# Kernel optimization log

Measured on AMD Instinct MI355X. Metric: run time of the kernel, lower is better.

## Reference

```python
import jax, jax.numpy as jnp
import numpy as np

N, M, BS = 32, 64, 512
ALPHA, BETA = 1.0, 1.0


def setup_inputs() -> dict:
    key = jax.random.key(0)
    k1, k2, k3, k4 = jax.random.split(key, 4)
    q = jax.random.normal(k1, (BS, N), jnp.float32)
    b = jax.random.normal(k2, (BS, M), jnp.float32)
    A0 = jax.random.normal(k3, (N, N), jnp.float32)
    P = A0 @ A0.T / N + jnp.eye(N, dtype=jnp.float32)  # SPD cost matrix
    H = jax.random.normal(k4, (M, N), jnp.float32) / jnp.sqrt(jnp.float32(N))
    return {"q": q, "b": b, "P": P, "H": H, "iters": 1000}


def reference(q, b, P, H, iters):
    m = H.shape[0]
    # Pinv-applied quantities via solve (matches torch.linalg.solve / pinv usage)
    Pinv_q = jnp.linalg.solve(P, q.T).T                 # (bs, n)
    D = H @ jnp.linalg.solve(P, H.T)                    # (m, m) = H P^-1 H^T
    # dummy preconditioner: scaled identity keeping the operator nonexpansive
    lam_max = jnp.linalg.eigvalsh(D)[-1]
    tD = (BETA / lam_max) * jnp.eye(m, dtype=q.dtype)   # (m, m)
    mu = ((H @ Pinv_q.T).T - b) @ tD.T                  # (bs, m)
    tDD = tD @ D
    I = jnp.eye(m, dtype=q.dtype)
    A = jnp.block([[tDD, tD],
                   [-2.0 * ALPHA * tDD + I, I - 2.0 * ALPHA * tD]])  # (2m, 2m)
    B = jnp.concatenate([mu, -2.0 * ALPHA * mu], axis=1)             # (bs, 2m)
    Hinv = jnp.linalg.pinv(H)                            # (n, m)
    X0 = jnp.zeros((q.shape[0], 2 * m), q.dtype)

    def step(X, _):
        X = X @ A.T + B
        X = X.at[:, m:].set(jax.nn.relu(X[:, m:]))       # in-place ReLU on dual half
        return X, X

    _, ys = jax.lax.scan(step, X0, None, length=iters)   # (iters, bs, 2m)
    Xs = jnp.concatenate([X0[None], ys], axis=0).transpose(1, 0, 2)  # (bs, iters+1, 2m)
    # primal_sols[k] = Hinv @ (X_k[m:] - b)
    primal_sols = jnp.einsum('nm,bkm->bkn', Hinv, Xs[:, :, m:] - b[:, None, :])
    return Xs, primal_sols
```

## Files before the change

### kernel.cpp

```cpp
#include <hip/hip_runtime.h>
#include <math.h>

#define BATCH 512
#define ITERS 1000
#define PLEN 25
#define PHASES 40

typedef float f32x2 __attribute__((ext_vector_type(2)));
typedef float f32x4 __attribute__((ext_vector_type(4)));

__device__ __forceinline__ float rdlane(float v, int l) {
  return __int_as_float(__builtin_amdgcn_readlane(__float_as_int(v), l));
}
__device__ __forceinline__ f32x2 fma2(f32x2 a, f32x2 b, f32x2 c) {
#if __has_builtin(__builtin_elementwise_fma)
  return __builtin_elementwise_fma(a, b, c);
#else
  f32x2 r; r.x = fmaf(a.x, b.x, c.x); r.y = fmaf(a.y, b.y, c.y); return r;
#endif
}

#define GJ32_REG(g)                                            \
  _Pragma("unroll")                                            \
  for (int k = 0; k < 32; ++k) {                               \
    float inv = 1.0f / rdlane(g[k], k);                        \
    g[k] *= inv;                                               \
    _Pragma("unroll")                                          \
    for (int ii = 0; ii < 32; ++ii) {                          \
      if (ii == k) continue;                                   \
      float f = rdlane(g[ii], k);                              \
      g[ii] = fmaf(-f, g[k], g[ii]);                           \
    }                                                          \
  }

__global__ __launch_bounds__(128, 1)
void fused_kernel(const float* __restrict__ q,
                  const float* __restrict__ bmat,
                  const float* __restrict__ P,
                  const float* __restrict__ H,
                  float* __restrict__ Xs,
                  float* __restrict__ out2) {
  __shared__ __align__(16) float stage[2112];
  __shared__ __align__(16) float X1R[2][PLEN][64];
  __shared__ __align__(16) float X2R[2][PLEN][64];

  const int tid = threadIdx.x;
  const int wv = tid >> 6;
  const int lane = tid & 63;
  const int row = blockIdx.x;
  const int i = lane & 31, h = lane >> 5;

  float hreg[32];
  {
    const f32x4* hp = (const f32x4*)(H + lane * 32);
    #pragma unroll
    for (int j4 = 0; j4 < 8; ++j4) {
      f32x4 t = hp[j4];
      hreg[4*j4+0] = t.x; hreg[4*j4+1] = t.y; hreg[4*j4+2] = t.z; hreg[4*j4+3] = t.w;
    }
  }
  const float bl = bmat[row * 64 + lane];

  float dcol[64]; float s = 0.f, mu = 0.f;
  f32x2 hv2[16];
  float* Xp = Xs + (size_t)row * (ITERS + 1) * 128;
  float* ob = out2 + (size_t)row * (ITERS + 1) * 32;

  if (wv == 1) {
    #pragma unroll
    for (int j = 0; j < 32; ++j) stage[lane * 33 + j] = hreg[j];
  }
  __syncthreads();
  float gB[32];
  if (wv == 1) {
    float htc[64];
    #pragma unroll
    for (int m = 0; m < 64; ++m) htc[m] = stage[m * 33 + i];
    #pragma unroll
    for (int r = 0; r < 32; ++r) {
      float a0 = 0.f, a1 = 0.f;
      #pragma unroll
      for (int m = 0; m < 64; m += 2) {
        a0 = fmaf(rdlane(hreg[r], m),     htc[m],     a0);
        a1 = fmaf(rdlane(hreg[r], m + 1), htc[m + 1], a1);
      }
      float hth = a0 + a1;
      gB[r] = (lane < 32) ? hth : (((lane - 32) == r) ? 1.0f : 0.0f);
    }
    GJ32_REG(gB)
  }
  __syncthreads();
  if (wv == 1) {
    #pragma unroll
    for (int r = 0; r < 32; ++r) {
      float a0 = 0.f, a1 = 0.f;
      #pragma unroll
      for (int c = 0; c < 32; c += 2) {
        a0 = fmaf(rdlane(gB[r], 32 + c),     hreg[c],     a0);
        a1 = fmaf(rdlane(gB[r], 32 + c + 1), hreg[c + 1], a1);
      }
      stage[r * 66 + lane] = a0 + a1;
    }
  }
  __syncthreads();
  if (wv == 1) {
    #pragma unroll
    for (int t = 0; t < 16; ++t)
      hv2[t] = *(const f32x2*)&stage[i * 66 + 32 * h + 2 * t];
  }

  if (wv == 0) {
    float pht[32], acc;
    {
      float g[32];
      #pragma unroll
      for (int r = 0; r < 32; ++r) {
        float pv = P[r * 32 + i];
        g[r] = (lane < 32) ? pv : (((lane - 32) == r) ? 1.0f : 0.0f);
      }
      GJ32_REG(g)
      #pragma unroll
      for (int r = 0; r < 32; ++r) {
        float a0 = 0.f, a1 = 0.f;
        #pragma unroll
        for (int j = 0; j < 32; j += 2) {
          a0 = fmaf(rdlane(g[r], 32 + j),     hreg[j],     a0);
          a1 = fmaf(rdlane(g[r], 32 + j + 1), hreg[j + 1], a1);
        }
        pht[r] = a0 + a1;
      }
    }
    {
      const float* qp = q + row * 32;
      float a0 = 0.f, a1 = 0.f;
      #pragma unroll
      for (int r = 0; r < 32; r += 2) {
        a0 = fmaf(qp[r],     pht[r],     a0);
        a1 = fmaf(qp[r + 1], pht[r + 1], a1);
      }
      acc = a0 + a1;
    }
    #pragma unroll
    for (int r = 0; r < 64; ++r) {
      float a0 = 0.f, a1 = 0.f;
      #pragma unroll
      for (int j = 0; j < 32; j += 2) {
        a0 = fmaf(rdlane(hreg[j],     r), pht[j],     a0);
        a1 = fmaf(rdlane(hreg[j + 1], r), pht[j + 1], a1);
      }
      dcol[r] = a0 + a1;
    }
    {
      float ecol[64];
      #pragma unroll
      for (int r = 0; r < 64; ++r) {
        float a0 = 0.f, a1 = 0.f;
        #pragma unroll
        for (int c = 0; c < 64; c += 2) {
          a0 = fmaf(rdlane(dcol[r], c),     dcol[c],     a0);
          a1 = fmaf(rdlane(dcol[r], c + 1), dcol[c + 1], a1);
        }
        ecol[r] = a0 + a1;
      }
      float v = 1.0f + 0.017f * (float)lane;
      #pragma unroll 1
      for (int t = 0; t < 112; ++t) {
        float a0 = 0.f, a1 = 0.f, a2 = 0.f, a3 = 0.f;
        #pragma unroll
        for (int c = 0; c < 64; c += 4) {
          a0 = fmaf(ecol[c+0], rdlane(v, c+0), a0);
          a1 = fmaf(ecol[c+1], rdlane(v, c+1), a1);
          a2 = fmaf(ecol[c+2], rdlane(v, c+2), a2);
          a3 = fmaf(ecol[c+3], rdlane(v, c+3), a3);
        }
        v = (a0 + a1) + (a2 + a3);
        if ((t & 7) == 7) {
          float n2 = v * v;
          #pragma unroll
          for (int m = 1; m < 64; m <<= 1) n2 += __shfl_xor(n2, m);
          v *= 1.0f / sqrtf(n2);
        }
      }
      float a0 = 0.f, a1 = 0.f, a2 = 0.f, a3 = 0.f;
      #pragma unroll
      for (int c = 0; c < 64; c += 4) {
        a0 = fmaf(dcol[c+0], rdlane(v, c+0), a0);
        a1 = fmaf(dcol[c+1], rdlane(v, c+1), a1);
        a2 = fmaf(dcol[c+2], rdlane(v, c+2), a2);
        a3 = fmaf(dcol[c+3], rdlane(v, c+3), a3);
      }
      float w = (a0 + a1) + (a2 + a3);
      float num = w * v, den = v * v;
      #pragma unroll
      for (int m = 1; m < 64; m <<= 1) {
        num += __shfl_xor(num, m);
        den += __shfl_xor(den, m);
      }
      s = den / num;
    }
    mu = s * (acc - bl);
    #pragma unroll
    for (int r = 0; r < 64; ++r) dcol[r] *= s;
  }

  float x1 = 0.f, x2 = 0.f;
  #pragma unroll 1
  for (int p = 0; p < PHASES; ++p) {
    if (wv == 0) {
      float* rx1 = &X1R[p & 1][0][0];
      float* rx2 = &X2R[p & 1][0][0];
      #pragma unroll 1
      for (int u = 0; u < PLEN; ++u) {
        float a0 = 0.f, a1 = 0.f, a2 = 0.f, a3 = 0.f;
        #pragma unroll
        for (int j8 = 0; j8 < 64; j8 += 8) {
          float b0 = rdlane(x1, j8+0), b1 = rdlane(x1, j8+1);
          float b2 = rdlane(x1, j8+2), b3 = rdlane(x1, j8+3);
          float b4 = rdlane(x1, j8+4), b5 = rdlane(x1, j8+5);
          float b6 = rdlane(x1, j8+6), b7 = rdlane(x1, j8+7);
          a0 = fmaf(dcol[j8+0], b0, a0);
          a1 = fmaf(dcol[j8+1], b1, a1);
          a2 = fmaf(dcol[j8+2], b2, a2);
          a3 = fmaf(dcol[j8+3], b3, a3);
          a0 = fmaf(dcol[j8+4], b4, a0);
          a1 = fmaf(dcol[j8+5], b5, a1);
          a2 = fmaf(dcol[j8+6], b6, a2);
          a3 = fmaf(dcol[j8+7], b7, a3);
        }
        float x1n = ((a0 + a1) + (a2 + a3)) + fmaf(s, x2, mu);
        float x2n = fmaxf(fmaf(-2.0f, x1n, x1 + x2), 0.f);
        rx1[u * 64 + lane] = x1n;
        rx2[u * 64 + lane] = x2n - bl;
        x1 = x1n; x2 = x2n;
      }
    } else {
      if (p == 0) {
        Xp[lane] = 0.f;
        Xp[64 + lane] = 0.f;
        f32x2 pa = {0.f, 0.f}, pb = {0.f, 0.f};
        #pragma unroll
        for (int t = 0; t < 8; ++t) {
          f32x2 ta, tb;
          ta.x = -__shfl(bl, 32*h + 4*t + 0, 64);
          ta.y = -__shfl(bl, 32*h + 4*t + 1, 64);
          tb.x = -__shfl(bl, 32*h + 4*t + 2, 64);
          tb.y = -__shfl(bl, 32*h + 4*t + 3, 64);
          pa = fma2(hv2[2*t],     ta, pa);
          pb = fma2(hv2[2*t + 1], tb, pb);
        }
        float pr = (pa.x + pa.y) + (pb.x + pb.y);
        pr += __shfl_xor(pr, 32);
        if (h == 0) ob[i] = pr;
      } else {
        const float* rx1 = &X1R[(p - 1) & 1][0][0];
        const float* rx2 = &X2R[(p - 1) & 1][0][0];
        const int k0 = PLEN * (p - 1) + 1;
        float* Xk = Xp + (size_t)k0 * 128;
        float* obk = ob + (size_t)k0 * 32;
        #pragma unroll 1
        for (int u = 0; u < PLEN; ++u) {
          float x1v = rx1[u * 64 + lane];
          float x2mb = rx2[u * 64 + lane];
          Xk[u * 128 + lane] = x1v;
          Xk[u * 128 + 64 + lane] = x2mb + bl;
          const f32x4* tp = (const f32x4*)(rx2 + u * 64 + h * 32);
          f32x2 pa = {0.f, 0.f}, pb = {0.f, 0.f};
          #pragma unroll
          for (int t = 0; t < 8; ++t) {
            f32x4 tv = tp[t];
            pa = fma2(hv2[2*t],     tv.xy, pa);
            pb = fma2(hv2[2*t + 1], tv.zw, pb);
          }
          float pr = (pa.x + pa.y) + (pb.x + pb.y);
          pr += __shfl_xor(pr, 32);
          if (h == 0) obk[u * 32 + i] = pr;
        }
      }
    }
    __syncthreads();
  }

  if (wv == 1) {
    const float* rx1 = &X1R[1][0][0];
    const float* rx2 = &X2R[1][0][0];
    const int k0 = PLEN * (PHASES - 1) + 1;
    float* Xk = Xp + (size_t)k0 * 128;
    float* obk = ob + (size_t)k0 * 32;
    #pragma unroll 1
    for (int u = 0; u < PLEN; ++u) {
      float x1v = rx1[u * 64 + lane];
      float x2mb = rx2[u * 64 + lane];
      Xk[u * 128 + lane] = x1v;
      Xk[u * 128 + 64 + lane] = x2mb + bl;
      const f32x4* tp = (const f32x4*)(rx2 + u * 64 + h * 32);
      f32x2 pa = {0.f, 0.f}, pb = {0.f, 0.f};
      #pragma unroll
      for (int t = 0; t < 8; ++t) {
        f32x4 tv = tp[t];
        pa = fma2(hv2[2*t],     tv.xy, pa);
        pb = fma2(hv2[2*t + 1], tv.zw, pb);
      }
      float pr = (pa.x + pa.y) + (pb.x + pb.y);
      pr += __shfl_xor(pr, 32);
      if (h == 0) obk[u * 32 + i] = pr;
    }
  }
}

extern "C" void kernel_launch(void* const* d_in, const int* in_sizes, int n_in,
                              void* d_out, int out_size, void* d_ws, size_t ws_size,
                              hipStream_t stream) {
  (void)in_sizes; (void)n_in; (void)out_size; (void)d_ws; (void)ws_size;
  const float* q = (const float*)d_in[0];
  const float* b = (const float*)d_in[1];
  const float* P = (const float*)d_in[2];
  const float* H = (const float*)d_in[3];
  float* Xs = (float*)d_out;
  float* out2 = Xs + (size_t)BATCH * (ITERS + 1) * 128;

  fused_kernel<<<BATCH, 128, 0, stream>>>(q, b, P, H, Xs, out2);
}
```

Baseline: 611.9 us.

## Process two batch rows per block, interleaving their serial recurrences

Each block now handles two batch rows and launches BATCH/2 blocks. The compute wave interleaves the two independent 1000-step recurrences so their readlane and FMA chains can hide each other's latency. The setup work (the Gauss-Jordan inverse and D) is also amortised over two rows. In exchange the grid is halved to 256 blocks, which can underfill the GPU's compute units, and each serial step now does twice the readlanes, so time per step may roughly double.

```diff
diff --git a/kernel.cpp b/kernel.cpp
--- a/kernel.cpp
+++ b/kernel.cpp
@@ -33,6 +33,26 @@
     }                                                          \
   }
 
+#define CONSUME25(rx1, rx2, Xk, obk, blv)                      \
+  _Pragma("unroll 1")                                          \
+  for (int u = 0; u < PLEN; ++u) {                             \
+    float x1v  = (rx1)[u * 64 + lane];                         \
+    float x2mb = (rx2)[u * 64 + lane];                         \
+    (Xk)[u * 128 + lane] = x1v;                                \
+    (Xk)[u * 128 + 64 + lane] = x2mb + (blv);                  \
+    const f32x4* tp = (const f32x4*)((rx2) + u * 64 + h * 32); \
+    f32x2 pa = {0.f, 0.f}, pb = {0.f, 0.f};                    \
+    _Pragma("unroll")                                          \
+    for (int t = 0; t < 8; ++t) {                              \
+      f32x4 tv = tp[t];                                        \
+      pa = fma2(hv2[2*t],     tv.xy, pa);                      \
+      pb = fma2(hv2[2*t + 1], tv.zw, pb);                      \
+    }                                                          \
+    float pr = (pa.x + pa.y) + (pb.x + pb.y);                  \
+    pr += __shfl_xor(pr, 32);                                  \
+    if (h == 0) (obk)[u * 32 + i] = pr;                        \
+  }
+
 __global__ __launch_bounds__(128, 1)
 void fused_kernel(const float* __restrict__ q,
                   const float* __restrict__ bmat,
@@ -41,13 +61,13 @@
                   float* __restrict__ Xs,
                   float* __restrict__ out2) {
   __shared__ __align__(16) float stage[2112];
-  __shared__ __align__(16) float X1R[2][PLEN][64];
-  __shared__ __align__(16) float X2R[2][PLEN][64];
+  __shared__ __align__(16) float X1R[2][2][PLEN][64];
+  __shared__ __align__(16) float X2R[2][2][PLEN][64];
 
   const int tid = threadIdx.x;
   const int wv = tid >> 6;
   const int lane = tid & 63;
-  const int row = blockIdx.x;
+  const int r0 = blockIdx.x * 2;
   const int i = lane & 31, h = lane >> 5;
 
   float hreg[32];
@@ -59,12 +79,15 @@
       hreg[4*j4+0] = t.x; hreg[4*j4+1] = t.y; hreg[4*j4+2] = t.z; hreg[4*j4+3] = t.w;
     }
   }
-  const float bl = bmat[row * 64 + lane];
-
-  float dcol[64]; float s = 0.f, mu = 0.f;
+  const float bla = bmat[r0 * 64 + lane];
+  const float blb = bmat[r0 * 64 + 64 + lane];
+
+  float dcol[64]; float s = 0.f, mua = 0.f, mub = 0.f;
   f32x2 hv2[16];
-  float* Xp = Xs + (size_t)row * (ITERS + 1) * 128;
-  float* ob = out2 + (size_t)row * (ITERS + 1) * 32;
+  float* Xpa = Xs + (size_t)r0 * (ITERS + 1) * 128;
+  float* Xpb = Xpa + (size_t)(ITERS + 1) * 128;
+  float* oba = out2 + (size_t)r0 * (ITERS + 1) * 32;
+  float* obb = oba + (size_t)(ITERS + 1) * 32;
 
   if (wv == 1) {
     #pragma unroll
@@ -110,7 +133,7 @@
   }
 
   if (wv == 0) {
-    float pht[32], acc;
+    float pht[32], acca, accb;
     {
       float g[32];
       #pragma unroll
@@ -131,14 +154,18 @@
       }
     }
     {
-      const float* qp = q + row * 32;
-      float a0 = 0.f, a1 = 0.f;
+      const float* qa = q + r0 * 32;
+      const float* qb = qa + 32;
+      float a0 = 0.f, a1 = 0.f, b0 = 0.f, b1 = 0.f;
       #pragma unroll
       for (int r = 0; r < 32; r += 2) {
-        a0 = fmaf(qp[r],     pht[r],     a0);
-        a1 = fmaf(qp[r + 1], pht[r + 1], a1);
-      }
-      acc = a0 + a1;
+        a0 = fmaf(qa[r],     pht[r],     a0);
+        a1 = fmaf(qa[r + 1], pht[r + 1], a1);
+        b0 = fmaf(qb[r],     pht[r],     b0);
+        b1 = fmaf(qb[r + 1], pht[r + 1], b1);
+      }
+      acca = a0 + a1;
+      accb = b0 + b1;
     }
     #pragma unroll
     for (int r = 0; r < 64; ++r) {
@@ -198,112 +225,115 @@
       }
       s = den / num;
     }
-    mu = s * (acc - bl);
+    mua = s * (acca - bla);
+    mub = s * (accb - blb);
     #pragma unroll
     for (int r = 0; r < 64; ++r) dcol[r] *= s;
   }
 
-  float x1 = 0.f, x2 = 0.f;
+  float x1a = 0.f, x2a = 0.f, x1b = 0.f, x2b = 0.f;
   #pragma unroll 1
   for (int p = 0; p < PHASES; ++p) {
     if (wv == 0) {
-      float* rx1 = &X1R[p & 1][0][0];
-      float* rx2 = &X2R[p & 1][0][0];
+      float* rx1a = &X1R[p & 1][0][0][0];
+      float* rx2a = &X2R[p & 1][0][0][0];
+      float* rx1b = &X1R[p & 1][1][0][0];
+      float* rx2b = &X2R[p & 1][1][0][0];
       #pragma unroll 1
       for (int u = 0; u < PLEN; ++u) {
+        float ta = fmaf(s, x2a, mua), tb = fmaf(s, x2b, mub);
         float a0 = 0.f, a1 = 0.f, a2 = 0.f, a3 = 0.f;
+        float c0 = 0.f, c1 = 0.f, c2 = 0.f, c3 = 0.f;
         #pragma unroll
         for (int j8 = 0; j8 < 64; j8 += 8) {
-          float b0 = rdlane(x1, j8+0), b1 = rdlane(x1, j8+1);
-          float b2 = rdlane(x1, j8+2), b3 = rdlane(x1, j8+3);
-          float b4 = rdlane(x1, j8+4), b5 = rdlane(x1, j8+5);
-          float b6 = rdlane(x1, j8+6), b7 = rdlane(x1, j8+7);
-          a0 = fmaf(dcol[j8+0], b0, a0);
-          a1 = fmaf(dcol[j8+1], b1, a1);
-          a2 = fmaf(dcol[j8+2], b2, a2);
-          a3 = fmaf(dcol[j8+3], b3, a3);
-          a0 = fmaf(dcol[j8+4], b4, a0);
-          a1 = fmaf(dcol[j8+5], b5, a1);
-          a2 = fmaf(dcol[j8+6], b6, a2);
-          a3 = fmaf(dcol[j8+7], b7, a3);
-        }
-        float x1n = ((a0 + a1) + (a2 + a3)) + fmaf(s, x2, mu);
-        float x2n = fmaxf(fmaf(-2.0f, x1n, x1 + x2), 0.f);
-        rx1[u * 64 + lane] = x1n;
-        rx2[u * 64 + lane] = x2n - bl;
-        x1 = x1n; x2 = x2n;
+          float pa0 = rdlane(x1a, j8+0), pa1 = rdlane(x1a, j8+1);
+          float pa2 = rdlane(x1a, j8+2), pa3 = rdlane(x1a, j8+3);
+          float pa4 = rdlane(x1a, j8+4), pa5 = rdlane(x1a, j8+5);
+          float pa6 = rdlane(x1a, j8+6), pa7 = rdlane(x1a, j8+7);
+          float pb0 = rdlane(x1b, j8+0), pb1 = rdlane(x1b, j8+1);
+          float pb2 = rdlane(x1b, j8+2), pb3 = rdlane(x1b, j8+3);
+          float pb4 = rdlane(x1b, j8+4), pb5 = rdlane(x1b, j8+5);
+          float pb6 = rdlane(x1b, j8+6), pb7 = rdlane(x1b, j8+7);
+          a0 = fmaf(dcol[j8+0], pa0, a0);
+          c0 = fmaf(dcol[j8+0], pb0, c0);
+          a1 = fmaf(dcol[j8+1], pa1, a1);
+          c1 = fmaf(dcol[j8+1], pb1, c1);
+          a2 = fmaf(dcol[j8+2], pa2, a2);
+          c2 = fmaf(dcol[j8+2], pb2, c2);
+          a3 = fmaf(dcol[j8+3], pa3, a3);
+          c3 = fmaf(dcol[j8+3], pb3, c3);
+          a0 = fmaf(dcol[j8+4], pa4, a0);
+          c0 = fmaf(dcol[j8+4], pb4, c0);
+          a1 = fmaf(dcol[j8+5], pa5, a1);
+          c1 = fmaf(dcol[j8+5], pb5, c1);
+          a2 = fmaf(dcol[j8+6], pa6, a2);
+          c2 = fmaf(dcol[j8+6], pb6, c2);
+          a3 = fmaf(dcol[j8+7], pa7, a3);
+          c3 = fmaf(dcol[j8+7], pb7, c3);
+        }
+        float x1na = ((a0 + a1) + (a2 + a3)) + ta;
+        float x1nb = ((c0 + c1) + (c2 + c3)) + tb;
+        float x2na = fmaxf(fmaf(-2.0f, x1na, x1a + x2a), 0.f);
+        float x2nb = fmaxf(fmaf(-2.0f, x1nb, x1b + x2b), 0.f);
+        rx1a[u * 64 + lane] = x1na;
+        rx2a[u * 64 + lane] = x2na - bla;
+        rx1b[u * 64 + lane] = x1nb;
+        rx2b[u * 64 + lane] = x2nb - blb;
+        x1a = x1na; x2a = x2na; x1b = x1nb; x2b = x2nb;
       }
     } else {
       if (p == 0) {
-        Xp[lane] = 0.f;
-        Xp[64 + lane] = 0.f;
-        f32x2 pa = {0.f, 0.f}, pb = {0.f, 0.f};
-        #pragma unroll
-        for (int t = 0; t < 8; ++t) {
-          f32x2 ta, tb;
-          ta.x = -__shfl(bl, 32*h + 4*t + 0, 64);
-          ta.y = -__shfl(bl, 32*h + 4*t + 1, 64);
-          tb.x = -__shfl(bl, 32*h + 4*t + 2, 64);
-          tb.y = -__shfl(bl, 32*h + 4*t + 3, 64);
-          pa = fma2(hv2[2*t],     ta, pa);
-          pb = fma2(hv2[2*t + 1], tb, pb);
-        }
-        float pr = (pa.x + pa.y) + (pb.x + pb.y);
-        pr += __shfl_xor(pr, 32);
-        if (h == 0) ob[i] = pr;
-      } else {
-        const float* rx1 = &X1R[(p - 1) & 1][0][0];
-        const float* rx2 = &X2R[(p - 1) & 1][0][0];
-        const int k0 = PLEN * (p - 1) + 1;
-        float* Xk = Xp + (size_t)k0 * 128;
-        float* obk = ob + (size_t)k0 * 32;
-        #pragma unroll 1
-        for (int u = 0; u < PLEN; ++u) {
-          float x1v = rx1[u * 64 + lane];
-          float x2mb = rx2[u * 64 + lane];
-          Xk[u * 128 + lane] = x1v;
-          Xk[u * 128 + 64 + lane] = x2mb + bl;
-          const f32x4* tp = (const f32x4*)(rx2 + u * 64 + h * 32);
+        Xpa[lane] = 0.f; Xpa[64 + lane] = 0.f;
+        Xpb[lane] = 0.f; Xpb[64 + lane] = 0.f;
+        {
           f32x2 pa = {0.f, 0.f}, pb = {0.f, 0.f};
           #pragma unroll
           for (int t = 0; t < 8; ++t) {
-            f32x4 tv = tp[t];
-            pa = fma2(hv2[2*t],     tv.xy, pa);
-            pb = fma2(hv2[2*t + 1], tv.zw, pb);
+            f32x2 ta, tb;
+            ta.x = -__shfl(bla, 32*h + 4*t + 0, 64);
+            ta.y = -__shfl(bla, 32*h + 4*t + 1, 64);
+            tb.x = -__shfl(bla, 32*h + 4*t + 2, 64);
+            tb.y = -__shfl(bla, 32*h + 4*t + 3, 64);
+            pa = fma2(hv2[2*t],     ta, pa);
+            pb = fma2(hv2[2*t + 1], tb, pb);
           }
           float pr = (pa.x + pa.y) + (pb.x + pb.y);
           pr += __shfl_xor(pr, 32);
-          if (h == 0) obk[u * 32 + i] = pr;
-        }
+          if (h == 0) oba[i] = pr;
+        }
+        {
+          f32x2 pa = {0.f, 0.f}, pb = {0.f, 0.f};
+          #pragma unroll
+          for (int t = 0; t < 8; ++t) {
+            f32x2 ta, tb;
+            ta.x = -__shfl(blb, 32*h + 4*t + 0, 64);
+            ta.y = -__shfl(blb, 32*h + 4*t + 1, 64);
+            tb.x = -__shfl(blb, 32*h + 4*t + 2, 64);
+            tb.y = -__shfl(blb, 32*h + 4*t + 3, 64);
+            pa = fma2(hv2[2*t],     ta, pa);
+            pb = fma2(hv2[2*t + 1], tb, pb);
+          }
+          float pr = (pa.x + pa.y) + (pb.x + pb.y);
+          pr += __shfl_xor(pr, 32);
+          if (h == 0) obb[i] = pr;
+        }
+      } else {
+        const int k0 = PLEN * (p - 1) + 1;
+        CONSUME25(&X1R[(p - 1) & 1][0][0][0], &X2R[(p - 1) & 1][0][0][0],
+                  Xpa + (size_t)k0 * 128, oba + (size_t)k0 * 32, bla)
+        CONSUME25(&X1R[(p - 1) & 1][1][0][0], &X2R[(p - 1) & 1][1][0][0],
+                  Xpb + (size_t)k0 * 128, obb + (size_t)k0 * 32, blb)
       }
     }
     __syncthreads();
   }
 
   if (wv == 1) {
-    const float* rx1 = &X1R[1][0][0];
-    const float* rx2 = &X2R[1][0][0];
     const int k0 = PLEN * (PHASES - 1) + 1;
-    float* Xk = Xp + (size_t)k0 * 128;
-    float* obk = ob + (size_t)k0 * 32;
-    #pragma unroll 1
-    for (int u = 0; u < PLEN; ++u) {
-      float x1v = rx1[u * 64 + lane];
-      float x2mb = rx2[u * 64 + lane];
-      Xk[u * 128 + lane] = x1v;
-      Xk[u * 128 + 64 + lane] = x2mb + bl;
-      const f32x4* tp = (const f32x4*)(rx2 + u * 64 + h * 32);
-      f32x2 pa = {0.f, 0.f}, pb = {0.f, 0.f};
-      #pragma unroll
-      for (int t = 0; t < 8; ++t) {
-        f32x4 tv = tp[t];
-        pa = fma2(hv2[2*t],     tv.xy, pa);
-        pb = fma2(hv2[2*t + 1], tv.zw, pb);
-      }
-      float pr = (pa.x + pa.y) + (pb.x + pb.y);
-      pr += __shfl_xor(pr, 32);
-      if (h == 0) obk[u * 32 + i] = pr;
-    }
+    CONSUME25(&X1R[1][0][0][0], &X2R[1][0][0][0],
+              Xpa + (size_t)k0 * 128, oba + (size_t)k0 * 32, bla)
+    CONSUME25(&X1R[1][1][0][0], &X2R[1][1][0][0],
+              Xpb + (size_t)k0 * 128, obb + (size_t)k0 * 32, blb)
   }
 }
 
@@ -318,5 +348,5 @@
   float* Xs = (float*)d_out;
   float* out2 = Xs + (size_t)BATCH * (ITERS + 1) * 128;
 
-  fused_kernel<<<BATCH, 128, 0, stream>>>(q, b, P, H, Xs, out2);
+  fused_kernel<<<BATCH / 2, 128, 0, stream>>>(q, b, P, H, Xs, out2);
 }
```

Result: slower. 958.5 us (+56.6%).
